# Optimization experiments

Hardware: AMD Instinct MI355X
Metric: run time of the kernel (lower is better)

Reference implementation:

```python
import jax, jax.numpy as jnp
import numpy as np

N = 50000      # nodes
E = 800000     # edges (before self-loops)
D_IN = 256     # input feature dim
H = 4          # attention heads
C = 32         # per-head channels
HID = H * C    # 128, concat output dim
BN_EPS = 1e-5


def setup_inputs() -> dict:
    key = jax.random.key(0)
    ks = jax.random.split(key, 24)
    inp = {}
    inp["x"] = jax.random.normal(ks[0], (N, D_IN), jnp.float32)
    inp["edge_index"] = jax.random.randint(ks[1], (2, E), 0, N, jnp.int32)
    # layer 1 GATConv params
    inp["W1"] = jax.random.normal(ks[2], (D_IN, HID), jnp.float32) * (2.0 / (D_IN + HID)) ** 0.5
    inp["att_src1"] = jax.random.normal(ks[3], (H, C), jnp.float32) * 0.1
    inp["att_dst1"] = jax.random.normal(ks[4], (H, C), jnp.float32) * 0.1
    inp["bias1"] = jnp.zeros((HID,), jnp.float32)
    # layer 1 BatchNorm (eval mode)
    inp["gamma1"] = 1.0 + 0.1 * jax.random.normal(ks[5], (HID,), jnp.float32)
    inp["beta1"] = 0.1 * jax.random.normal(ks[6], (HID,), jnp.float32)
    inp["mean1"] = 0.1 * jax.random.normal(ks[7], (HID,), jnp.float32)
    inp["var1"] = 0.5 + jax.random.uniform(ks[8], (HID,), jnp.float32)
    # layer 2 GATConv params
    inp["W2"] = jax.random.normal(ks[9], (HID, HID), jnp.float32) * (2.0 / (HID + HID)) ** 0.5
    inp["att_src2"] = jax.random.normal(ks[10], (H, C), jnp.float32) * 0.1
    inp["att_dst2"] = jax.random.normal(ks[11], (H, C), jnp.float32) * 0.1
    inp["bias2"] = jnp.zeros((HID,), jnp.float32)
    # layer 2 BatchNorm (eval mode)
    inp["gamma2"] = 1.0 + 0.1 * jax.random.normal(ks[12], (HID,), jnp.float32)
    inp["beta2"] = 0.1 * jax.random.normal(ks[13], (HID,), jnp.float32)
    inp["mean2"] = 0.1 * jax.random.normal(ks[14], (HID,), jnp.float32)
    inp["var2"] = 0.5 + jax.random.uniform(ks[15], (HID,), jnp.float32)
    return inp


def _gat_layer(x, src, dst, W, att_src, att_dst, bias):
    # x: [N, D]; src/dst: [Etot] with self-loops already appended
    h = (x @ W).reshape(N, H, C)                       # [N, H, C]
    a_s = jnp.einsum("nhc,hc->nh", h, att_src)         # [N, H]
    a_d = jnp.einsum("nhc,hc->nh", h, att_dst)         # [N, H]
    e = jax.nn.leaky_relu(a_s[src] + a_d[dst], 0.2)    # [Etot, H]
    # edge softmax over incoming edges of each destination node
    m = jax.ops.segment_max(e, dst, num_segments=N)    # [N, H]
    ex = jnp.exp(e - m[dst])                           # [Etot, H]
    den = jax.ops.segment_sum(ex, dst, num_segments=N) # [N, H]
    alpha = ex / (den[dst] + 1e-16)                    # [Etot, H]
    out = jax.ops.segment_sum(h[src] * alpha[:, :, None], dst, num_segments=N)
    return out.reshape(N, HID) + bias                  # concat heads + bias


def _bn_eval(x, gamma, beta, mean, var):
    return (x - mean) * (gamma * jax.lax.rsqrt(var + BN_EPS)) + beta


def reference(x, edge_index, W1, att_src1, att_dst1, bias1, gamma1, beta1, mean1, var1,
              W2, att_src2, att_dst2, bias2, gamma2, beta2, mean2, var2):
    loop = jnp.arange(N, dtype=edge_index.dtype)
    src = jnp.concatenate([edge_index[0], loop])  # PyG GATConv adds self-loops
    dst = jnp.concatenate([edge_index[1], loop])
    h = _gat_layer(x, src, dst, W1, att_src1, att_dst1, bias1)
    h = jax.nn.relu(_bn_eval(h, gamma1, beta1, mean1, var1))  # dropout = identity (eval)
    h = _gat_layer(h, src, dst, W2, att_src2, att_dst2, bias2)
    h = jax.nn.relu(_bn_eval(h, gamma2, beta2, mean2, var2))
    return h
```

## Files before the change

### kernel.cpp

```cpp
#include <hip/hip_runtime.h>
#include <math.h>

#define N_NODES 50000
#define EDGES   800000
#define ETOT    (EDGES + N_NODES)
#define HID     128
#define NH      4

typedef __attribute__((ext_vector_type(8))) short short8;
typedef __attribute__((ext_vector_type(4))) float floatx4;

__device__ inline unsigned short f2bf(float f) {
    unsigned int u = __float_as_uint(f);
    u = u + 0x7FFFu + ((u >> 16) & 1u);
    return (unsigned short)(u >> 16);
}

#define NB 391
#define BCAP 2688
#define CHUNK 4096
#define BIN_BLOCKS ((ETOT + CHUNK - 1) / CHUNK)

__device__ __forceinline__ void bin_scatter_body(int* histL, int bid,
                                                 const int* __restrict__ ei,
                                                 int* __restrict__ cursor,
                                                 int* __restrict__ binned) {
    int t = threadIdx.x;
    for (int b = t; b < NB; b += 256) histL[b] = 0;
    __syncthreads();
    int base = bid * CHUNK;
#pragma unroll
    for (int j = 0; j < 16; j++) {
        int e = base + j * 256 + t;
        if (e < ETOT) {
            int d = (e < EDGES) ? ei[EDGES + e] : (e - EDGES);
            atomicAdd(&histL[d >> 7], 1);
        }
    }
    __syncthreads();
    for (int b = t; b < NB; b += 256) {
        int c = histL[b];
        histL[b] = c ? (b * BCAP + atomicAdd(&cursor[b], c)) : 0;
    }
    __syncthreads();
#pragma unroll
    for (int j = 0; j < 16; j++) {
        int e = base + j * 256 + t;
        if (e < ETOT) {
            int s, d;
            if (e < EDGES) { s = ei[e]; d = ei[EDGES + e]; }
            else           { s = d = e - EDGES; }
            int bb = d >> 7;
            int pos = atomicAdd(&histL[bb], 1);
            if (pos < (bb + 1) * BCAP)
                binned[pos] = (s << 7) | (d & 127);
        }
    }
}

__global__ __launch_bounds__(256) void bin_finalize_kernel(const int* __restrict__ binned,
                                                           const int* __restrict__ cursor,
                                                           int* __restrict__ starts,
                                                           int* __restrict__ degs,
                                                           int* __restrict__ csr) {
    __shared__ int histN[128];
    __shared__ int excl[128];
    int b = blockIdx.x, t = threadIdx.x;
    int n0 = b << 7;
    int S = b * BCAP;
    int cnt = cursor[b];
    if (cnt > BCAP) cnt = BCAP;
    if (t < 128) histN[t] = 0;
    __syncthreads();
    for (int j = t; j < cnt; j += 256)
        atomicAdd(&histN[binned[S + j] & 127], 1);
    __syncthreads();
    int v = (t < 128) ? histN[t] : 0;
    if (t < 128) excl[t] = v;
    __syncthreads();
    for (int off = 1; off < 128; off <<= 1) {
        int x = 0, add = 0;
        if (t < 128) { x = excl[t]; if (t >= off) add = excl[t - off]; }
        __syncthreads();
        if (t < 128) excl[t] = x + add;
        __syncthreads();
    }
    if (t < 128) {
        int ex = excl[t] - v;
        int n = n0 + t;
        if (n < N_NODES) { starts[n] = S + ex; degs[n] = v; }
        histN[t] = ex;
    }
    __syncthreads();
    for (int j = t; j < cnt; j += 256) {
        int e = binned[S + j];
        int pos = atomicAdd(&histN[e & 127], 1);
        csr[S + pos] = e >> 7;
    }
}

__global__ void wtrans_coef_kernel(const float* __restrict__ W1, const float* __restrict__ W2,
                                   unsigned short* __restrict__ Wt1, unsigned short* __restrict__ Wt2,
                                   const float* __restrict__ b1, const float* __restrict__ g1,
                                   const float* __restrict__ be1, const float* __restrict__ mn1,
                                   const float* __restrict__ vr1,
                                   const float* __restrict__ b2, const float* __restrict__ g2,
                                   const float* __restrict__ be2, const float* __restrict__ mn2,
                                   const float* __restrict__ vr2, float* __restrict__ coef) {
    int i = blockIdx.x * 256 + threadIdx.x;
    if (i < 256 * 128) { int k = i >> 7, n = i & 127; Wt1[n * 256 + k] = f2bf(W1[i]); }
    if (i < 128 * 128) { int k = i >> 7, n = i & 127; Wt2[n * 128 + k] = f2bf(W2[i]); }
    if (blockIdx.x == 0) {
        int t = threadIdx.x;
        if (t < 128) {
            float sc = g1[t] * rsqrtf(vr1[t] + 1e-5f);
            coef[t]       = sc;
            coef[128 + t] = be1[t] + (b1[t] - mn1[t]) * sc;
        } else {
            int c = t - 128;
            float sc = g2[c] * rsqrtf(vr2[c] + 1e-5f);
            coef[256 + c] = sc;
            coef[384 + c] = be2[c] + (b2[c] - mn2[c]) * sc;
        }
    }
}

#define GR   64
#define KC   64
#define PADK 88
#define PADH 136

union Smem {
    struct { unsigned short Xs[GR][PADK]; unsigned short Ws[HID][PADK]; } s;
    unsigned short Hs[GR][PADH];
};

template<bool XBF16>
__device__ __forceinline__ void gemm_att_body(Smem& sm, int bid,
                                              const void* __restrict__ Xv,
                                              const unsigned short* __restrict__ Wt,
                                              const float* __restrict__ att_src,
                                              const float* __restrict__ att_dst,
                                              unsigned short* __restrict__ Hout,
                                              float* __restrict__ aS,
                                              float* __restrict__ aD, int K) {
    int t = threadIdx.x, lane = t & 63, w = t >> 6;
    int quad = lane >> 4, nl = lane & 15;
    int rowBase = bid * GR;

    floatx4 acc[8];
    floatx4 zero = {0.f, 0.f, 0.f, 0.f};
#pragma unroll
    for (int b = 0; b < 8; b++) acc[b] = zero;

    const float*          Xf = (const float*)Xv;
    const unsigned short* Xb = (const unsigned short*)Xv;

    for (int k0 = 0; k0 < K; k0 += KC) {
#pragma unroll
        for (int it = 0; it < 2; it++) {
            int s5 = t + it * 256;
            int row = s5 >> 3, kg = s5 & 7;
            int gr = rowBase + row;
            unsigned short tmp[8];
            if (XBF16) {
                uint4 v = make_uint4(0, 0, 0, 0);
                if (gr < N_NODES) v = *(const uint4*)&Xb[(unsigned)(gr * K + k0 + kg * 8)];
                *(uint4*)tmp = v;
            } else {
                float4 v0 = make_float4(0, 0, 0, 0), v1 = v0;
                if (gr < N_NODES) {
                    const float* p = &Xf[(unsigned)(gr * K + k0 + kg * 8)];
                    v0 = *(const float4*)p;
                    v1 = *(const float4*)(p + 4);
                }
                tmp[0] = f2bf(v0.x); tmp[1] = f2bf(v0.y); tmp[2] = f2bf(v0.z); tmp[3] = f2bf(v0.w);
                tmp[4] = f2bf(v1.x); tmp[5] = f2bf(v1.y); tmp[6] = f2bf(v1.z); tmp[7] = f2bf(v1.w);
            }
            *(uint4*)&sm.s.Xs[row][kg * 8] = *(uint4*)tmp;
        }
#pragma unroll
        for (int it = 0; it < 4; it++) {
            int s5 = t + it * 256;
            int n = s5 >> 3, kg = s5 & 7;
            *(uint4*)&sm.s.Ws[n][kg * 8] = *(const uint4*)&Wt[(unsigned)(n * K + k0 + kg * 8)];
        }
        __syncthreads();
#pragma unroll
        for (int ks = 0; ks < 2; ks++) {
            int kb = ks * 32 + quad * 8;
            short8 a0 = *(const short8*)&sm.s.Xs[w * 16 + nl][kb];
#pragma unroll
            for (int ct = 0; ct < 8; ct++) {
                short8 b = *(const short8*)&sm.s.Ws[ct * 16 + nl][kb];
                acc[ct] = __builtin_amdgcn_mfma_f32_16x16x32_bf16(a0, b, acc[ct], 0, 0, 0);
            }
        }
        __syncthreads();
    }

#pragma unroll
    for (int ct = 0; ct < 8; ct++)
#pragma unroll
        for (int r = 0; r < 4; r++)
            sm.Hs[w * 16 + quad * 4 + r][ct * 16 + nl] = f2bf(acc[ct][r]);

    float asv[8], adv[8];
    {
        const float* ap = &att_src[nl * 8];
        const float* dp = &att_dst[nl * 8];
        *(float4*)&asv[0] = *(const float4*)ap;  *(float4*)&asv[4] = *(const float4*)(ap + 4);
        *(float4*)&adv[0] = *(const float4*)dp;  *(float4*)&adv[4] = *(const float4*)(dp + 4);
    }
    int hd = nl >> 2;
#pragma unroll
    for (int it = 0; it < 4; it++) {
        int rl = w * 16 + it * 4 + quad;
        int grow = rowBase + rl;
        uint4 v = *(const uint4*)&sm.Hs[rl][nl * 8];
        float f[8];
        f[0] = __uint_as_float(v.x << 16); f[1] = __uint_as_float(v.x & 0xffff0000u);
        f[2] = __uint_as_float(v.y << 16); f[3] = __uint_as_float(v.y & 0xffff0000u);
        f[4] = __uint_as_float(v.z << 16); f[5] = __uint_as_float(v.z & 0xffff0000u);
        f[6] = __uint_as_float(v.w << 16); f[7] = __uint_as_float(v.w & 0xffff0000u);
        float ds = 0.f, dd = 0.f;
#pragma unroll
        for (int j = 0; j < 8; j++) {
            ds = fmaf(f[j], asv[j], ds);
            dd = fmaf(f[j], adv[j], dd);
        }
        ds += __shfl_xor(ds, 1); ds += __shfl_xor(ds, 2);
        dd += __shfl_xor(dd, 1); dd += __shfl_xor(dd, 2);
        if (grow < N_NODES) {
            *(uint4*)&Hout[(unsigned)(grow * HID + nl * 8)] = v;
            if ((nl & 3) == 0) { aS[grow * 4 + hd] = ds; aD[grow * 4 + hd] = dd; }
        }
    }
}

__global__ __launch_bounds__(256) void fused_scatter_gemm1(
        const int* __restrict__ ei, int* __restrict__ cursor, int* __restrict__ binned,
        const float* __restrict__ x, const unsigned short* __restrict__ Wt1,
        const float* __restrict__ att_src, const float* __restrict__ att_dst,
        unsigned short* __restrict__ Hout, float* __restrict__ aS, float* __restrict__ aD) {
    __shared__ Smem sm;
    __shared__ int histL[NB];
    if (blockIdx.x < BIN_BLOCKS) {
        bin_scatter_body(histL, blockIdx.x, ei, cursor, binned);
    } else {
        gemm_att_body<false>(sm, blockIdx.x - BIN_BLOCKS, x, Wt1, att_src, att_dst,
                             Hout, aS, aD, 256);
    }
}

template<bool XBF16>
__global__ __launch_bounds__(256) void gemm_att_kernel(const void* __restrict__ Xv,
                                                       const unsigned short* __restrict__ Wt,
                                                       const float* __restrict__ att_src,
                                                       const float* __restrict__ att_dst,
                                                       unsigned short* __restrict__ Hout,
                                                       float* __restrict__ aS,
                                                       float* __restrict__ aD, int K) {
    __shared__ Smem sm;
    gemm_att_body<XBF16>(sm, blockIdx.x, Xv, Wt, att_src, att_dst, Hout, aS, aD, K);
}

#define ECAP 64

__device__ __forceinline__ void prefetchR(uint4 (&buf)[4], int sregr, const char* hbase,
                                          int sBase, int l16b) {
#pragma unroll
    for (int u = 0; u < 4; u++) {
        int se = __builtin_amdgcn_ds_bpermute(sBase | (u << 2), sregr);
        buf[u] = *(const uint4*)(hbase + (((long)se) << 8) + l16b);
    }
}

__device__ __forceinline__ void consumeR(const uint4 (&buf)[4], float xrr, int aBase,
                                         float (&acc)[8]) {
#pragma unroll
    for (int u = 0; u < 4; u++) {
        float au = __uint_as_float((unsigned)__builtin_amdgcn_ds_bpermute(
                        aBase | (u << 2), (int)__float_as_uint(xrr)));
        uint4 v = buf[u];
        acc[0] = fmaf(__uint_as_float(v.x << 16),         au, acc[0]);
        acc[1] = fmaf(__uint_as_float(v.x & 0xffff0000u), au, acc[1]);
        acc[2] = fmaf(__uint_as_float(v.y << 16),         au, acc[2]);
        acc[3] = fmaf(__uint_as_float(v.y & 0xffff0000u), au, acc[3]);
        acc[4] = fmaf(__uint_as_float(v.z << 16),         au, acc[4]);
        acc[5] = fmaf(__uint_as_float(v.z & 0xffff0000u), au, acc[5]);
        acc[6] = fmaf(__uint_as_float(v.w << 16),         au, acc[6]);
        acc[7] = fmaf(__uint_as_float(v.w & 0xffff0000u), au, acc[7]);
    }
}

template<bool OUTBF16>
__global__ __launch_bounds__(256) void gather_kernel(const unsigned short* __restrict__ hfeat,
                                                     const float* __restrict__ a_s,
                                                     const float* __restrict__ a_d,
                                                     const int* __restrict__ starts,
                                                     const int* __restrict__ degs,
                                                     const int* __restrict__ csr,
                                                     const float* __restrict__ coefA,
                                                     const float* __restrict__ coefB,
                                                     void* __restrict__ outv) {
    int t = threadIdx.x, lane = t & 63, ws = t >> 6;
    int h = lane >> 4, l16 = lane & 15;
    int n = blockIdx.x * 4 + ws;
    int start = starts[n];
    int deg = degs[n];
    float adh = a_d[(unsigned)(n * 4 + h)];
    const char* hbase = (const char*)hfeat;
    int sBase = lane & 48;
    int aBase = ((lane & 12) << 4) | sBase;
    int l16b = l16 << 4;

    int sreg[4];
#pragma unroll
    for (int it = 0; it < 4; it++) {
        int j = l16 + it * 16;
        sreg[it] = (j < deg) ? csr[start + j] : 0;
    }
    float e[4];
#pragma unroll
    for (int it = 0; it < 4; it++) {
        int j = l16 + it * 16;
        e[it] = -1e30f;
        if (j < deg) {
            float as = a_s[(unsigned)(sreg[it] * 4 + h)];
            float v = as + adh;
            e[it] = v > 0.f ? v : 0.2f * v;
        }
    }

    int cap = deg < ECAP ? deg : ECAP;
    uint4 vA[4], vB[4];
    prefetchR(vA, sreg[0], hbase, sBase, l16b);
    if (cap > 16) prefetchR(vB, sreg[1], hbase, sBase, l16b);

    float m = fmaxf(fmaxf(e[0], e[1]), fmaxf(e[2], e[3]));
    for (int j = ECAP + l16; j < deg; j += 16) {
        int s = csr[start + j];
        float as = a_s[(unsigned)(s * 4 + h)];
        float v = as + adh; v = v > 0.f ? v : 0.2f * v;
        m = fmaxf(m, v);
    }
#pragma unroll
    for (int off = 1; off < 16; off <<= 1) m = fmaxf(m, __shfl_xor(m, off));

    float x[4];
    float d = 0.f;
#pragma unroll
    for (int it = 0; it < 4; it++) { x[it] = __expf(e[it] - m); d += x[it]; }
    for (int j = ECAP + l16; j < deg; j += 16) {
        int s = csr[start + j];
        float as = a_s[(unsigned)(s * 4 + h)];
        float v = as + adh; v = v > 0.f ? v : 0.2f * v;
        d += __expf(v - m);
    }
#pragma unroll
    for (int off = 1; off < 16; off <<= 1) d += __shfl_xor(d, off);
    float rd = 1.0f / (d + 1e-16f);
    float xr[4];
#pragma unroll
    for (int it = 0; it < 4; it++) xr[it] = x[it] * rd;

    float acc[8];
#pragma unroll
    for (int j = 0; j < 8; j++) acc[j] = 0.f;
    consumeR(vA, xr[0], aBase, acc);
    if (cap > 16) {
        if (cap > 32) prefetchR(vA, sreg[2], hbase, sBase, l16b);
        consumeR(vB, xr[1], aBase, acc);
        if (cap > 32) {
            if (cap > 48) prefetchR(vB, sreg[3], hbase, sBase, l16b);
            consumeR(vA, xr[2], aBase, acc);
            if (cap > 48) consumeR(vB, xr[3], aBase, acc);
        }
    }
    if (deg > ECAP) {
        int hh = l16 >> 2;
        int gB = (lane & 12) << 4;
        float mB  = __uint_as_float((unsigned)__builtin_amdgcn_ds_bpermute(gB, (int)__float_as_uint(m)));
        float rdB = __uint_as_float((unsigned)__builtin_amdgcn_ds_bpermute(gB, (int)__float_as_uint(rd)));
        float adhB = a_d[(unsigned)(n * 4 + hh)];
        for (int j = ECAP; j < deg; j++) {
            int s = csr[start + j];
            float asv = a_s[(unsigned)(s * 4 + hh)];
            float v2 = asv + adhB; v2 = v2 > 0.f ? v2 : 0.2f * v2;
            float al = __expf(v2 - mB) * rdB;
            uint4 v = *(const uint4*)(hbase + (((long)s) << 8) + l16b);
            acc[0] = fmaf(__uint_as_float(v.x << 16),         al, acc[0]);
            acc[1] = fmaf(__uint_as_float(v.x & 0xffff0000u), al, acc[1]);
            acc[2] = fmaf(__uint_as_float(v.y << 16),         al, acc[2]);
            acc[3] = fmaf(__uint_as_float(v.y & 0xffff0000u), al, acc[3]);
            acc[4] = fmaf(__uint_as_float(v.z << 16),         al, acc[4]);
            acc[5] = fmaf(__uint_as_float(v.z & 0xffff0000u), al, acc[5]);
            acc[6] = fmaf(__uint_as_float(v.w << 16),         al, acc[6]);
            acc[7] = fmaf(__uint_as_float(v.w & 0xffff0000u), al, acc[7]);
        }
    }

#pragma unroll
    for (int j = 0; j < 8; j++) {
        acc[j] += __shfl_xor(acc[j], 16);
        acc[j] += __shfl_xor(acc[j], 32);
    }

    int g = lane >> 4;
    float o0 = acc[0], o1 = acc[1];
    if (g == 1) { o0 = acc[2]; o1 = acc[3]; }
    if (g == 2) { o0 = acc[4]; o1 = acc[5]; }
    if (g == 3) { o0 = acc[6]; o1 = acc[7]; }
    int c = (l16 << 3) + (g << 1);
    float2 cA = *(const float2*)&coefA[c];
    float2 cB = *(const float2*)&coefB[c];
    float r0 = fmaxf(fmaf(o0, cA.x, cB.x), 0.f);
    float r1 = fmaxf(fmaf(o1, cA.y, cB.y), 0.f);
    unsigned oidx = (unsigned)(n * 64 + (l16 << 2) + g);
    if (OUTBF16) {
        unsigned int pk = (unsigned int)f2bf(r0) | ((unsigned int)f2bf(r1) << 16);
        ((unsigned int*)outv)[oidx] = pk;
    } else {
        ((float2*)outv)[oidx] = make_float2(r0, r1);
    }
}

extern "C" void kernel_launch(void* const* d_in, const int* in_sizes, int n_in,
                              void* d_out, int out_size, void* d_ws, size_t ws_size,
                              hipStream_t stream) {
    const float* x    = (const float*)d_in[0];
    const int*   ei   = (const int*)d_in[1];
    const float* W1   = (const float*)d_in[2];
    const float* as1  = (const float*)d_in[3];
    const float* ad1  = (const float*)d_in[4];
    const float* b1   = (const float*)d_in[5];
    const float* g1   = (const float*)d_in[6];
    const float* be1  = (const float*)d_in[7];
    const float* mn1  = (const float*)d_in[8];
    const float* vr1  = (const float*)d_in[9];
    const float* W2   = (const float*)d_in[10];
    const float* as2  = (const float*)d_in[11];
    const float* ad2  = (const float*)d_in[12];
    const float* b2   = (const float*)d_in[13];
    const float* g2   = (const float*)d_in[14];
    const float* be2  = (const float*)d_in[15];
    const float* mn2  = (const float*)d_in[16];
    const float* vr2  = (const float*)d_in[17];
    float* out = (float*)d_out;

    unsigned short* hb  = (unsigned short*)d_ws;
    unsigned short* x2b = hb + (size_t)N_NODES * HID;
    unsigned short* Wt1 = x2b + (size_t)N_NODES * HID;
    unsigned short* Wt2 = Wt1 + 128 * 256;
    float* aS    = (float*)(Wt2 + 128 * 128);
    float* aD    = aS + N_NODES * NH;
    float* coef  = aD + N_NODES * NH;
    int* cursor  = (int*)(coef + 512);
    int* starts  = cursor + NB;
    int* degs    = starts + N_NODES;
    int* binned  = degs + N_NODES;
    int* csr     = binned + NB * BCAP;

    hipMemsetAsync(cursor, 0, NB * sizeof(int), stream);
    wtrans_coef_kernel<<<128, 256, 0, stream>>>(W1, W2, Wt1, Wt2,
                                                b1, g1, be1, mn1, vr1,
                                                b2, g2, be2, mn2, vr2, coef);

    int gemmGrid = (N_NODES + GR - 1) / GR;
    int nodeGrid = N_NODES / 4;

    fused_scatter_gemm1<<<BIN_BLOCKS + gemmGrid, 256, 0, stream>>>(
        ei, cursor, binned, x, Wt1, as1, ad1, hb, aS, aD);
    bin_finalize_kernel<<<NB, 256, 0, stream>>>(binned, cursor, starts, degs, csr);
    gather_kernel<true><<<nodeGrid, 256, 0, stream>>>(hb, aS, aD, starts, degs, csr,
                                                      coef, coef + 128, (void*)x2b);
    gemm_att_kernel<true><<<gemmGrid, 256, 0, stream>>>(x2b, Wt2, as2, ad2, hb, aS, aD, 128);
    gather_kernel<false><<<nodeGrid, 256, 0, stream>>>(hb, aS, aD, starts, degs, csr,
                                                       coef + 256, coef + 384, (void*)out);
}
```

Baseline: 248.1 us.

## Split layer-1 GEMM across scatter and finalize launches and drop cursor memset

```diff
diff --git a/kernel.cpp b/kernel.cpp
--- a/kernel.cpp
+++ b/kernel.cpp
@@ -20,6 +20,7 @@
 #define BCAP 2688
 #define CHUNK 4096
 #define BIN_BLOCKS ((ETOT + CHUNK - 1) / CHUNK)
+#define G1A 391
 
 __device__ __forceinline__ void bin_scatter_body(int* histL, int bid,
                                                  const int* __restrict__ ei,
@@ -58,14 +59,13 @@
     }
 }
 
-__global__ __launch_bounds__(256) void bin_finalize_kernel(const int* __restrict__ binned,
-                                                           const int* __restrict__ cursor,
-                                                           int* __restrict__ starts,
-                                                           int* __restrict__ degs,
-                                                           int* __restrict__ csr) {
-    __shared__ int histN[128];
-    __shared__ int excl[128];
-    int b = blockIdx.x, t = threadIdx.x;
+__device__ __forceinline__ void bin_finalize_body(int* histN, int* excl, int b,
+                                                  const int* __restrict__ binned,
+                                                  const int* __restrict__ cursor,
+                                                  int* __restrict__ starts,
+                                                  int* __restrict__ degs,
+                                                  int* __restrict__ csr) {
+    int t = threadIdx.x;
     int n0 = b << 7;
     int S = b * BCAP;
     int cnt = cursor[b];
@@ -106,8 +106,10 @@
                                    const float* __restrict__ vr1,
                                    const float* __restrict__ b2, const float* __restrict__ g2,
                                    const float* __restrict__ be2, const float* __restrict__ mn2,
-                                   const float* __restrict__ vr2, float* __restrict__ coef) {
+                                   const float* __restrict__ vr2, float* __restrict__ coef,
+                                   int* __restrict__ cursor) {
     int i = blockIdx.x * 256 + threadIdx.x;
+    if (i < NB) cursor[i] = 0;
     if (i < 256 * 128) { int k = i >> 7, n = i & 127; Wt1[n * 256 + k] = f2bf(W1[i]); }
     if (i < 128 * 128) { int k = i >> 7, n = i & 127; Wt2[n * 128 + k] = f2bf(W2[i]); }
     if (blockIdx.x == 0) {
@@ -238,7 +240,7 @@
     }
 }
 
-__global__ __launch_bounds__(256) void fused_scatter_gemm1(
+__global__ __launch_bounds__(256) void fused_scatter_gemm1a(
         const int* __restrict__ ei, int* __restrict__ cursor, int* __restrict__ binned,
         const float* __restrict__ x, const unsigned short* __restrict__ Wt1,
         const float* __restrict__ att_src, const float* __restrict__ att_dst,
@@ -249,6 +251,23 @@
         bin_scatter_body(histL, blockIdx.x, ei, cursor, binned);
     } else {
         gemm_att_body<false>(sm, blockIdx.x - BIN_BLOCKS, x, Wt1, att_src, att_dst,
+                             Hout, aS, aD, 256);
+    }
+}
+
+__global__ __launch_bounds__(256) void fused_finalize_gemm1b(
+        const int* __restrict__ binned, const int* __restrict__ cursor,
+        int* __restrict__ starts, int* __restrict__ degs, int* __restrict__ csr,
+        const float* __restrict__ x, const unsigned short* __restrict__ Wt1,
+        const float* __restrict__ att_src, const float* __restrict__ att_dst,
+        unsigned short* __restrict__ Hout, float* __restrict__ aS, float* __restrict__ aD) {
+    __shared__ Smem sm;
+    __shared__ int histN[128];
+    __shared__ int excl[128];
+    if (blockIdx.x < NB) {
+        bin_finalize_body(histN, excl, blockIdx.x, binned, cursor, starts, degs, csr);
+    } else {
+        gemm_att_body<false>(sm, blockIdx.x, x, Wt1, att_src, att_dst,
                              Hout, aS, aD, 256);
     }
 }
@@ -462,17 +481,17 @@
     int* binned  = degs + N_NODES;
     int* csr     = binned + NB * BCAP;
 
-    hipMemsetAsync(cursor, 0, NB * sizeof(int), stream);
     wtrans_coef_kernel<<<128, 256, 0, stream>>>(W1, W2, Wt1, Wt2,
                                                 b1, g1, be1, mn1, vr1,
-                                                b2, g2, be2, mn2, vr2, coef);
+                                                b2, g2, be2, mn2, vr2, coef, cursor);
 
     int gemmGrid = (N_NODES + GR - 1) / GR;
     int nodeGrid = N_NODES / 4;
 
-    fused_scatter_gemm1<<<BIN_BLOCKS + gemmGrid, 256, 0, stream>>>(
+    fused_scatter_gemm1a<<<BIN_BLOCKS + G1A, 256, 0, stream>>>(
         ei, cursor, binned, x, Wt1, as1, ad1, hb, aS, aD);
-    bin_finalize_kernel<<<NB, 256, 0, stream>>>(binned, cursor, starts, degs, csr);
+    fused_finalize_gemm1b<<<gemmGrid, 256, 0, stream>>>(
+        binned, cursor, starts, degs, csr, x, Wt1, as1, ad1, hb, aS, aD);
     gather_kernel<true><<<nodeGrid, 256, 0, stream>>>(hb, aS, aD, starts, degs, csr,
                                                       coef, coef + 128, (void*)x2b);
     gemm_att_kernel<true><<<gemmGrid, 256, 0, stream>>>(x2b, Wt2, as2, ad2, hb, aS, aD, 128);
```

Result: no change. 251.2 us (+1.2%).
